# Kernel tuning notes

Hardware: AMD Instinct MI355X
Metric: run time of the kernel (lower is better)

## Reference

```python
import jax, jax.numpy as jnp
from jax import lax
import numpy as np


def _conv(x, w, b, groups=1):
    # x: NCHW, w: OIHW, stride 1, SAME padding
    y = lax.conv_general_dilated(x, w, (1, 1), 'SAME',
                                 dimension_numbers=('NCHW', 'OIHW', 'NCHW'),
                                 feature_group_count=groups)
    return y + b[None, :, None, None]


def setup_inputs() -> dict:
    key = jax.random.key(0)
    ks = jax.random.split(key, 9)
    B, C, H, W, N, K = 8, 64, 256, 256, 10, 64
    f = lambda k, s, sc=0.05: jax.random.normal(k, s, dtype=jnp.float32) * sc
    return dict(
        x=jax.random.normal(ks[0], (B, C, H, W), dtype=jnp.float32),
        ln_g=jnp.ones((C,), jnp.float32), ln_b=jnp.zeros((C,), jnp.float32),
        conv3_w=f(ks[1], (C, C, 3, 3)), conv3_b=jnp.zeros((C,), jnp.float32),
        dw_w=f(ks[2], (C, 1, 3, 3)), dw_b=jnp.zeros((C,), jnp.float32),
        c1_w=f(ks[3], (C, C, 1, 1)), c1_b=jnp.zeros((C,), jnp.float32),
        c2_w=f(ks[4], (N, C, 1, 1)), c2_b=jnp.zeros((N,), jnp.float32),
        base=f(ks[5], (N, K, K), 1.0),
        up_w=f(ks[6], (K, C, 3, 3)), up_b=jnp.zeros((K,), jnp.float32),
        down_w=f(ks[7], (C, K, 3, 3)), down_b=jnp.zeros((C,), jnp.float32),
    )


def reference(x, ln_g, ln_b, conv3_w, conv3_b, dw_w, dw_b, c1_w, c1_b,
              c2_w, c2_b, base, up_w, up_b, down_w, down_b):
    eps = 1e-5
    # LayerNorm over channel dim (permute(0,2,3,1) -> LN(last) -> permute back)
    mu = jnp.mean(x, axis=1, keepdims=True)
    var = jnp.var(x, axis=1, keepdims=True)
    xn = (x - mu) / jnp.sqrt(var + eps) * ln_g[None, :, None, None] + ln_b[None, :, None, None]
    x1 = jax.nn.gelu(_conv(xn, conv3_w, conv3_b), approximate=False)
    # predict module: dwconv -> GAP -> 1x1 -> relu -> 1x1 -> softmax over N
    C = x.shape[1]
    p = _conv(x1, dw_w, dw_b, groups=C)
    p = jnp.mean(p, axis=(2, 3), keepdims=True)           # [B,C,1,1]
    p = jax.nn.relu(_conv(p, c1_w, c1_b))
    p = _conv(p, c2_w, c2_b)[:, :, 0, 0]                  # [B,N]
    w = jax.nn.softmax(p, axis=1)                         # [B,N]
    # blend N basis KxK matrices per sample
    Wm = jnp.einsum('bn,nkl->bkl', w, base)               # [B,K,K]
    xm = _conv(x1, up_w, up_b)                            # [B,K,H,W]
    B, K, H, Wd = xm.shape
    xm = jnp.einsum('bkl,bkm->blm', Wm, xm.reshape(B, K, H * Wd)).reshape(B, K, H, Wd)
    xm = _conv(xm, down_w, down_b)                        # [B,C,H,W]
    return x + xm
```

## Files before the change

### kernel.cpp

```cpp
#include <hip/hip_runtime.h>
#include <math.h>

constexpr int B = 8, C = 64, H = 256, W = 256, HWc = H * W, N = 10;

typedef short bf8 __attribute__((ext_vector_type(8)));
typedef float f4  __attribute__((ext_vector_type(4)));
typedef unsigned short ushort;

__device__ __forceinline__ ushort f2bf(float f) {
  unsigned u = __builtin_bit_cast(unsigned, f);
  unsigned r = (u + 0x7fffu + ((u >> 16) & 1u)) >> 16;
  return (ushort)r;
}
__device__ __forceinline__ float bf2f(ushort h) {
  unsigned u = ((unsigned)h) << 16;
  return __builtin_bit_cast(float, u);
}

__global__ __launch_bounds__(256) void ln_k(
    const float* __restrict__ x, const float* __restrict__ g,
    const float* __restrict__ bt, ushort* __restrict__ xn) {
  int pix = blockIdx.x * 256 + threadIdx.x;
  int b = blockIdx.y;
  const float* xp = x + (size_t)b * C * HWc + pix;
  float v[64];
  float s = 0.f, s2 = 0.f;
#pragma unroll
  for (int c = 0; c < 64; c++) {
    v[c] = xp[(size_t)c * HWc];
    s += v[c]; s2 += v[c] * v[c];
  }
  float mu = s * (1.f / 64);
  float var = s2 * (1.f / 64) - mu * mu;
  float rstd = rsqrtf(var + 1e-5f);
  ushort* op = xn + ((size_t)b * HWc + pix) * 64;
#pragma unroll
  for (int ch = 0; ch < 8; ch++) {
    union { ushort us[8]; int4 v4; } pk;
#pragma unroll
    for (int j = 0; j < 8; j++) {
      int c = ch * 8 + j;
      pk.us[j] = f2bf((v[c] - mu) * rstd * g[c] + bt[c]);
    }
    *reinterpret_cast<int4*>(op + ch * 8) = pk.v4;
  }
}

__global__ void prep_w(const float* __restrict__ w3, const float* __restrict__ wu,
                       const float* __restrict__ wd, ushort* __restrict__ frags) {
  int idx = blockIdx.x * 256 + threadIdx.x;
  if (idx >= 3 * 4608) return;
  int conv = idx / 4608, r = idx % 4608;
  int s = r >> 8, cf = (r >> 6) & 3, lane = r & 63;
  const float* w = (conv == 0) ? w3 : (conv == 1) ? wu : wd;
  int co = (cf << 4) + (lane & 15);
  int tap = s >> 1;
  ushort* o = frags + conv * 36864 + ((size_t)r) * 8;
#pragma unroll
  for (int j = 0; j < 8; j++) {
    int ci = ((s & 1) << 5) + ((lane >> 4) << 3) + j;
    o[j] = f2bf(w[(co * 64 + ci) * 9 + tap]);
  }
}

struct Stg { int4 v[6]; };

__device__ __forceinline__ void stage_load(
    Stg& s, const ushort* __restrict__ in, int b, int h0, int w0,
    int ch2, int tid) {
#pragma unroll
  for (int it = 0; it < 6; it++) {
    int idx = it * 256 + tid;
    int4 v = make_int4(0, 0, 0, 0);
    if (idx < 1296) {
      int pix = idx >> 2, ch = idx & 3;
      int r = pix / 18, c = pix % 18;
      int gh = h0 + r - 1, gw = w0 + c - 1;
      if (gh >= 0 && gh < H && gw >= 0 && gw < W)
        v = *reinterpret_cast<const int4*>(
            in + (((size_t)b * H + gh) * W + gw) * 64 + ch2 * 32 + ch * 8);
    }
    s.v[it] = v;
  }
}

__device__ __forceinline__ void stage_write(const Stg& s, char* lds, int tid) {
#pragma unroll
  for (int it = 0; it < 6; it++) {
    int idx = it * 256 + tid;
    if (idx < 1296) {
      int pix = idx >> 2, ch = idx & 3;
      int c = pix % 18;
      int off = ((pix << 6) + (ch << 4)) ^ (((c >> 1) & 3) << 4);
      *reinterpret_cast<int4*>(lds + off) = s.v[it];
    }
  }
}

__device__ __forceinline__ void compute_half(
    const char* lds, const bf8* __restrict__ wf, int ch2,
    int wave, int lm, int lk, f4 (&acc)[16]) {
#pragma unroll
  for (int dx = 0; dx < 3; dx++) {
    bf8 wb3[3];
#pragma unroll
    for (int dy = 0; dy < 3; dy++) {
      int s = ((dy * 3 + dx) << 1) | ch2;
      wb3[dy] = wf[(s * 4 + wave) * 64 + (lk << 4) + lm];
    }
    int lc = lm + dx;
    int swz = ((lc >> 1) & 3) << 4;
#pragma unroll
    for (int hf = 0; hf < 2; hf++) {
      bf8 a[10];
#pragma unroll
      for (int r = 0; r < 10; r++) {
        int row = hf * 8 + r;
        int off = (((row * 18 + lc) << 6) + (lk << 4)) ^ swz;
        a[r] = *reinterpret_cast<const bf8*>(lds + off);
      }
#pragma unroll
      for (int dy = 0; dy < 3; dy++)
#pragma unroll
        for (int f = 0; f < 8; f++)
          acc[hf * 8 + f] =
              __builtin_amdgcn_mfma_f32_16x16x32_bf16(a[f + dy], wb3[dy], acc[hf * 8 + f], 0, 0, 0);
    }
  }
}

__device__ __forceinline__ void red_at(
    float* ldsf, const float (&a)[8], float* __restrict__ Ssum,
    int b, int tid) {
  __syncthreads();
#pragma unroll
  for (int j = 0; j < 8; j++) ldsf[j * 256 + tid] = a[j];
  __syncthreads();
  if (tid < 64) {
    float s = 0.f;
#pragma unroll
    for (int kk = 0; kk < 32; kk++) s += ldsf[(tid & 7) * 256 + kk * 8 + (tid >> 3)];
    atomicAdd(&Ssum[b * 64 + tid], s);
  }
}

template <int ACT, int OM, int DOST>
__global__ __launch_bounds__(256, 2) void conv_mfma(
    const ushort* __restrict__ in, const ushort* __restrict__ wfrag,
    const float* __restrict__ bias, const float* __restrict__ resid,
    ushort* __restrict__ outb, float* __restrict__ outf,
    float* __restrict__ Ssum) {
  __shared__ char lds[2 * 20736];
  char* ldsA = lds;
  char* ldsB = lds + 20736;
  int tid = threadIdx.x;
  int b = blockIdx.z;
  int h0 = blockIdx.y * 16, w0 = blockIdx.x * 16;
  int wave = tid >> 6, lane = tid & 63;
  int lm = lane & 15, lk = lane >> 4;
  const bf8* wf = reinterpret_cast<const bf8*>(wfrag);

  f4 acc[16];
  {
    float bv = bias[(wave << 4) + lm];
    f4 ini = {bv, bv, bv, bv};
#pragma unroll
    for (int f = 0; f < 16; f++) acc[f] = ini;
  }

  {
    Stg s0;
    stage_load(s0, in, b, h0, w0, 0, tid);
    stage_write(s0, ldsA, tid);
    __syncthreads();
  }
  {
    Stg s1;
    stage_load(s1, in, b, h0, w0, 1, tid);
    compute_half(ldsA, wf, 0, wave, lm, lk, acc);
    stage_write(s1, ldsB, tid);
    __syncthreads();
  }
  compute_half(ldsB, wf, 1, wave, lm, lk, acc);

  float* ldsf = reinterpret_cast<float*>(lds);
  if (OM == 0) {
    float s8[8];
    if (DOST) {
#pragma unroll
      for (int j = 0; j < 8; j++) s8[j] = 0.f;
    }
    for (int h2 = 0; h2 < 2; h2++) {
      __syncthreads();
#pragma unroll
      for (int fr = 0; fr < 8; fr++) {
        int f = h2 * 8 + fr;
        int co = (wave << 4) + lm;
#pragma unroll
        for (int r = 0; r < 4; r++) {
          int p = (lk << 2) + r;
          ldsf[fr * 1024 + p * 64 + (co ^ ((p & 12) << 2))] = acc[f][r];
        }
      }
      __syncthreads();
#pragma unroll
      for (int i = 0; i < 4; i++) {
        int q2 = i * 256 + tid;
        int co8 = q2 & 7, p = (q2 >> 3) & 15, fr = q2 >> 7;
        int cb = (co8 * 8) ^ ((p & 12) << 2);
        f4 v0 = *reinterpret_cast<f4*>(&ldsf[fr * 1024 + p * 64 + cb]);
        f4 v1 = *reinterpret_cast<f4*>(&ldsf[fr * 1024 + p * 64 + cb + 4]);
        float vv[8] = {v0[0], v0[1], v0[2], v0[3], v1[0], v1[1], v1[2], v1[3]};
        union { ushort us[8]; int4 i4; } pk;
#pragma unroll
        for (int j = 0; j < 8; j++) {
          float v = vv[j];
          if (ACT) v = 0.5f * v * (1.f + erff(v * 0.70710678118654752f));
          if (DOST) s8[j] += v;
          pk.us[j] = f2bf(v);
        }
        *reinterpret_cast<int4*>(
            outb + (((size_t)b * H + h0 + h2 * 8 + fr) * W + w0 + p) * 64 + co8 * 8) = pk.i4;
      }
    }
    if (DOST) red_at(ldsf, s8, Ssum, b, tid);
  } else {
    for (int h2 = 0; h2 < 2; h2++) {
      __syncthreads();
      if ((wave >> 1) == h2) {
        int co32 = ((wave & 1) << 4) + lm;
#pragma unroll
        for (int f = 0; f < 16; f++) {
          int pxl = (f << 4) + (lk << 2);
          int pxs = pxl ^ ((co32 & 7) << 2);
          *reinterpret_cast<f4*>(&ldsf[co32 * 256 + pxs]) = acc[f];
        }
      }
      float4 rv[8];
#pragma unroll
      for (int i = 0; i < 8; i++) {
        int q2 = i * 256 + tid;
        int chunk = q2 & 63, co32 = q2 >> 6;
        int pq = chunk * 4;
        int co = h2 * 32 + co32;
        size_t o = ((size_t)(b * 64 + co)) * HWc +
                   (size_t)(h0 + (pq >> 4)) * W + w0 + (pq & 15);
        rv[i] = *reinterpret_cast<const float4*>(resid + o);
      }
      __syncthreads();
#pragma unroll
      for (int i = 0; i < 8; i++) {
        int q2 = i * 256 + tid;
        int chunk = q2 & 63, co32 = q2 >> 6;
        int pq = chunk * 4;
        int pxs = pq ^ ((co32 & 7) << 2);
        f4 v = *reinterpret_cast<f4*>(&ldsf[co32 * 256 + pxs]);
        int co = h2 * 32 + co32;
        size_t o = ((size_t)(b * 64 + co)) * HWc +
                   (size_t)(h0 + (pq >> 4)) * W + w0 + (pq & 15);
        float4 ov;
        ov.x = v[0] + rv[i].x; ov.y = v[1] + rv[i].y;
        ov.z = v[2] + rv[i].z; ov.w = v[3] + rv[i].w;
        *reinterpret_cast<float4*>(outf + o) = ov;
      }
    }
  }
}

__global__ __launch_bounds__(256, 2) void upmix_mfma(
    const ushort* __restrict__ in, const ushort* __restrict__ wfrag,
    const float* __restrict__ bias, const ushort* __restrict__ wmf,
    ushort* __restrict__ out) {
  __shared__ char ldsS[20736];
  __shared__ char ldsX[32768];
  int tid = threadIdx.x;
  int b = blockIdx.z;
  int h0 = blockIdx.y * 16, w0 = blockIdx.x * 16;
  int wave = tid >> 6, lane = tid & 63;
  int lm = lane & 15, lk = lane >> 4;
  const bf8* wf = reinterpret_cast<const bf8*>(wfrag);

  const bf8* wmb = reinterpret_cast<const bf8*>(wmf + (size_t)b * 4096);
  bf8 wm[2];
#pragma unroll
  for (int s = 0; s < 2; s++) wm[s] = wmb[(s * 4 + wave) * 64 + lane];

  f4 acc[16];
  {
    float bv = bias[(wave << 4) + lm];
    f4 ini = {bv, bv, bv, bv};
#pragma unroll
    for (int f = 0; f < 16; f++) acc[f] = ini;
  }

  {
    Stg s0;
    stage_load(s0, in, b, h0, w0, 0, tid);
    stage_write(s0, ldsS, tid);
    __syncthreads();
  }
  {
    Stg s1;
    stage_load(s1, in, b, h0, w0, 1, tid);
    compute_half(ldsS, wf, 0, wave, lm, lk, acc);
    stage_write(s1, ldsX, tid);
    __syncthreads();
  }
  compute_half(ldsX, wf, 1, wave, lm, lk, acc);
  __syncthreads();

#pragma unroll
  for (int f = 0; f < 16; f++) {
#pragma unroll
    for (int r = 0; r < 4; r++) {
      int pc = (lk << 2) + r;
      int pix = (f << 4) + pc;
      int off = ((pix << 7) + ((wave << 4) + lm) * 2) ^ ((pc & 7) << 4);
      *reinterpret_cast<ushort*>(ldsX + off) = f2bf(acc[f][r]);
    }
  }
  __syncthreads();

  f4 acc2[16];
#pragma unroll
  for (int f = 0; f < 16; f++) acc2[f] = (f4){0.f, 0.f, 0.f, 0.f};
#pragma unroll
  for (int s = 0; s < 2; s++) {
    int kbyte = ((s << 5) + (lk << 3)) << 1;
#pragma unroll
    for (int f = 0; f < 16; f++) {
      int off = ((((f << 4) + lm) << 7) + kbyte) ^ ((lm & 7) << 4);
      bf8 a = *reinterpret_cast<const bf8*>(ldsX + off);
      acc2[f] = __builtin_amdgcn_mfma_f32_16x16x32_bf16(a, wm[s], acc2[f], 0, 0, 0);
    }
  }

  float* ldsf = reinterpret_cast<float*>(ldsX);
  for (int h2 = 0; h2 < 2; h2++) {
    __syncthreads();
#pragma unroll
    for (int fr = 0; fr < 8; fr++) {
      int f = h2 * 8 + fr;
      int co = (wave << 4) + lm;
#pragma unroll
      for (int r = 0; r < 4; r++) {
        int p = (lk << 2) + r;
        ldsf[fr * 1024 + p * 64 + (co ^ ((p & 12) << 2))] = acc2[f][r];
      }
    }
    __syncthreads();
#pragma unroll
    for (int i = 0; i < 4; i++) {
      int q2 = i * 256 + tid;
      int co8 = q2 & 7, p = (q2 >> 3) & 15, fr = q2 >> 7;
      int cb = (co8 * 8) ^ ((p & 12) << 2);
      f4 v0 = *reinterpret_cast<f4*>(&ldsf[fr * 1024 + p * 64 + cb]);
      f4 v1 = *reinterpret_cast<f4*>(&ldsf[fr * 1024 + p * 64 + cb + 4]);
      float vv[8] = {v0[0], v0[1], v0[2], v0[3], v1[0], v1[1], v1[2], v1[3]};
      union { ushort us[8]; int4 i4; } pk;
#pragma unroll
      for (int j = 0; j < 8; j++) pk.us[j] = f2bf(vv[j]);
      *reinterpret_cast<int4*>(
          out + (((size_t)b * H + h0 + h2 * 8 + fr) * W + w0 + p) * 64 + co8 * 8) = pk.i4;
    }
  }
}

__global__ __launch_bounds__(256) void mlp_k(
    const ushort* __restrict__ x1, const float* __restrict__ Ssum,
    const float* __restrict__ dww, const float* __restrict__ dwb,
    const float* __restrict__ c1w, const float* __restrict__ c1b,
    const float* __restrict__ c2w, const float* __restrict__ c2b,
    const float* __restrict__ basep, ushort* __restrict__ wmf) {
  int b = blockIdx.x;
  int t = threadIdx.x;
  __shared__ float red[256];
  __shared__ float eg[4][64], corn[4][64];
  __shared__ float pm[64], p1[64], p2[16];
  const size_t bb = (size_t)b * HWc * 64;
#pragma unroll
  for (int st = 0; st < 4; st++) {
    float s = 0.f;
    for (int i = 0; i < 64; i++) {
      int idx = i * 256 + t;
      int pix = idx >> 6, c = idx & 63;
      size_t off;
      if (st == 0)      off = ((size_t)pix) * 64 + c;
      else if (st == 1) off = ((size_t)(H - 1) * W + pix) * 64 + c;
      else if (st == 2) off = ((size_t)pix * W) * 64 + c;
      else              off = ((size_t)pix * W + (W - 1)) * 64 + c;
      s += bf2f(x1[bb + off]);
    }
    red[t] = s;
    __syncthreads();
    if (t < 64) eg[st][t] = red[t] + red[t + 64] + red[t + 128] + red[t + 192];
    __syncthreads();
  }
  if (t < 64) {
    corn[0][t] = bf2f(x1[bb + t]);
    corn[1][t] = bf2f(x1[bb + ((size_t)(W - 1)) * 64 + t]);
    corn[2][t] = bf2f(x1[bb + ((size_t)(H - 1) * W) * 64 + t]);
    corn[3][t] = bf2f(x1[bb + ((size_t)(H - 1) * W + W - 1) * 64 + t]);
  }
  __syncthreads();
  if (t < 64) {
    float S = Ssum[b * 64 + t];
    float R0 = eg[0][t], Rh = eg[1][t], C0 = eg[2][t], Cw = eg[3][t];
    float X00 = corn[0][t], X0w = corn[1][t], Xh0 = corn[2][t], Xhw = corn[3][t];
    float acc = 0.f;
#pragma unroll
    for (int ky = 0; ky < 3; ky++)
#pragma unroll
      for (int kx = 0; kx < 3; kx++) {
        float T = S;
        if (ky == 2) T -= R0;
        if (ky == 0) T -= Rh;
        if (kx == 2) T -= C0;
        if (kx == 0) T -= Cw;
        if (ky == 2 && kx == 2) T += X00;
        if (ky == 2 && kx == 0) T += X0w;
        if (ky == 0 && kx == 2) T += Xh0;
        if (ky == 0 && kx == 0) T += Xhw;
        acc += dww[t * 9 + ky * 3 + kx] * T;
      }
    pm[t] = acc * (1.f / HWc) + dwb[t];
  }
  __syncthreads();
  if (t < 64) {
    float a = c1b[t];
    for (int ci = 0; ci < 64; ci++) a += pm[ci] * c1w[t * 64 + ci];
    p1[t] = fmaxf(a, 0.f);
  }
  __syncthreads();
  if (t < N) {
    float a2 = c2b[t];
    for (int ci = 0; ci < 64; ci++) a2 += p1[ci] * c2w[t * 64 + ci];
    p2[t] = a2;
  }
  __syncthreads();
  float m = -1e30f;
  for (int n = 0; n < N; n++) m = fmaxf(m, p2[n]);
  float ev[N], s = 0.f;
  for (int n = 0; n < N; n++) { ev[n] = expf(p2[n] - m); s += ev[n]; }
  float inv = 1.f / s;
  for (int idx = t; idx < 4096; idx += 256) {
    int j = idx & 7, lane = (idx >> 3) & 63, cf = (idx >> 9) & 3, s2 = idx >> 11;
    int k = (s2 << 5) + ((lane >> 4) << 3) + j;
    int l = (cf << 4) + (lane & 15);
    float acc = 0.f;
    for (int n = 0; n < N; n++) acc += ev[n] * inv * basep[n * 4096 + k * 64 + l];
    wmf[(size_t)b * 4096 + idx] = f2bf(acc);
  }
}

__global__ void zero_k(float* p, int n) {
  int i = blockIdx.x * 256 + threadIdx.x;
  if (i < n) p[i] = 0.f;
}

extern "C" void kernel_launch(void* const* d_in, const int* in_sizes, int n_in,
                              void* d_out, int out_size, void* d_ws, size_t ws_size,
                              hipStream_t stream) {
  const float* x       = (const float*)d_in[0];
  const float* ln_g    = (const float*)d_in[1];
  const float* ln_b    = (const float*)d_in[2];
  const float* conv3_w = (const float*)d_in[3];
  const float* conv3_b = (const float*)d_in[4];
  const float* dw_w    = (const float*)d_in[5];
  const float* dw_b    = (const float*)d_in[6];
  const float* c1_w    = (const float*)d_in[7];
  const float* c1_b    = (const float*)d_in[8];
  const float* c2_w    = (const float*)d_in[9];
  const float* c2_b    = (const float*)d_in[10];
  const float* basep   = (const float*)d_in[11];
  const float* up_w    = (const float*)d_in[12];
  const float* up_b    = (const float*)d_in[13];
  const float* down_w  = (const float*)d_in[14];
  const float* down_b  = (const float*)d_in[15];
  float* out = (float*)d_out;

  char* wsb = (char*)d_ws;
  size_t big = (size_t)B * HWc * 64 * sizeof(ushort);
  ushort* bufA   = (ushort*)wsb;
  ushort* bufB   = (ushort*)(wsb + big);
  ushort* wfrags = (ushort*)(wsb + 2 * big);
  ushort* wmfrag = (ushort*)(wsb + 2 * big + 3 * 36864 * 2);
  float*  Ssum   = (float*)(wsb + 2 * big + 3 * 36864 * 2 + 8 * 4096 * 2);

  prep_w<<<54, 256, 0, stream>>>(conv3_w, up_w, down_w, wfrags);
  zero_k<<<2, 256, 0, stream>>>(Ssum, B * 64);
  ln_k<<<dim3(HWc / 256, B), 256, 0, stream>>>(x, ln_g, ln_b, bufA);
  conv_mfma<1, 0, 1><<<dim3(16, 16, B), 256, 0, stream>>>(
      bufA, wfrags + 0 * 36864, conv3_b, nullptr, bufB, nullptr, Ssum);
  mlp_k<<<B, 256, 0, stream>>>(bufB, Ssum, dw_w, dw_b, c1_w, c1_b, c2_w, c2_b,
                               basep, wmfrag);
  upmix_mfma<<<dim3(16, 16, B), 256, 0, stream>>>(
      bufB, wfrags + 1 * 36864, up_b, wmfrag, bufA);
  conv_mfma<0, 1, 0><<<dim3(16, 16, B), 256, 0, stream>>>(
      bufA, wfrags + 2 * 36864, down_b, x, nullptr, out, Ssum);
}
```

Measured before the change: 311.1 us.

## Stage conv input tiles directly into LDS via global_load_lds with zero buffer

```diff
diff --git a/kernel.cpp b/kernel.cpp
--- a/kernel.cpp
+++ b/kernel.cpp
@@ -63,37 +63,27 @@
   }
 }
 
-struct Stg { int4 v[6]; };
-
-__device__ __forceinline__ void stage_load(
-    Stg& s, const ushort* __restrict__ in, int b, int h0, int w0,
-    int ch2, int tid) {
+typedef __attribute__((address_space(3))) unsigned lds_u32;
+typedef __attribute__((address_space(1))) const unsigned glb_u32;
+
+__device__ __forceinline__ void stage_gll(
+    char* ldsbuf, const ushort* __restrict__ in, const ushort* __restrict__ zbuf,
+    int b, int h0, int w0, int ch2, int tid) {
+  int wave = tid >> 6, lane = tid & 63;
 #pragma unroll
   for (int it = 0; it < 6; it++) {
-    int idx = it * 256 + tid;
-    int4 v = make_int4(0, 0, 0, 0);
-    if (idx < 1296) {
-      int pix = idx >> 2, ch = idx & 3;
-      int r = pix / 18, c = pix % 18;
-      int gh = h0 + r - 1, gw = w0 + c - 1;
-      if (gh >= 0 && gh < H && gw >= 0 && gw < W)
-        v = *reinterpret_cast<const int4*>(
-            in + (((size_t)b * H + gh) * W + gw) * 64 + ch2 * 32 + ch * 8);
-    }
-    s.v[it] = v;
-  }
-}
-
-__device__ __forceinline__ void stage_write(const Stg& s, char* lds, int tid) {
-#pragma unroll
-  for (int it = 0; it < 6; it++) {
-    int idx = it * 256 + tid;
-    if (idx < 1296) {
-      int pix = idx >> 2, ch = idx & 3;
-      int c = pix % 18;
-      int off = ((pix << 6) + (ch << 4)) ^ (((c >> 1) & 3) << 4);
-      *reinterpret_cast<int4*>(lds + off) = s.v[it];
-    }
+    int idx = it * 256 + wave * 64 + lane;
+    int pix = idx >> 2, ch = idx & 3;
+    int r = pix / 18, c = pix % 18;
+    int gh = h0 + r - 1, gw = w0 + c - 1;
+    int chs = ch ^ ((c >> 1) & 3);
+    bool ok = (idx < 1296) && (gh >= 0) && (gh < H) && (gw >= 0) && (gw < W);
+    const ushort* src = ok
+        ? in + (((size_t)b * H + gh) * W + gw) * 64 + ch2 * 32 + chs * 8
+        : zbuf;
+    char* dst = ldsbuf + (it * 256 + wave * 64) * 16;
+    __builtin_amdgcn_global_load_lds((glb_u32*)(const void*)src,
+                                     (lds_u32*)(void*)dst, 16, 0, 0);
   }
 }
 
@@ -128,6 +118,18 @@
     }
   }
 }
+
+#define STAGE_PIPELINE(bufA_, bufB_)                                      \
+  stage_gll(bufA_, in, zbuf, b, h0, w0, 0, tid);                          \
+  stage_gll(bufB_, in, zbuf, b, h0, w0, 1, tid);                          \
+  asm volatile("s_waitcnt vmcnt(6)" ::: "memory");                        \
+  __builtin_amdgcn_s_barrier();                                           \
+  __builtin_amdgcn_sched_barrier(0);                                      \
+  compute_half(bufA_, wf, 0, wave, lm, lk, acc);                          \
+  asm volatile("s_waitcnt vmcnt(0)" ::: "memory");                        \
+  __builtin_amdgcn_s_barrier();                                           \
+  __builtin_amdgcn_sched_barrier(0);                                      \
+  compute_half(bufB_, wf, 1, wave, lm, lk, acc);
 
 __device__ __forceinline__ void red_at(
     float* ldsf, const float (&a)[8], float* __restrict__ Ssum,
@@ -149,10 +151,10 @@
     const ushort* __restrict__ in, const ushort* __restrict__ wfrag,
     const float* __restrict__ bias, const float* __restrict__ resid,
     ushort* __restrict__ outb, float* __restrict__ outf,
-    float* __restrict__ Ssum) {
-  __shared__ char lds[2 * 20736];
+    float* __restrict__ Ssum, const ushort* __restrict__ zbuf) {
+  __shared__ char lds[2 * 24576];
   char* ldsA = lds;
-  char* ldsB = lds + 20736;
+  char* ldsB = lds + 24576;
   int tid = threadIdx.x;
   int b = blockIdx.z;
   int h0 = blockIdx.y * 16, w0 = blockIdx.x * 16;
@@ -168,20 +170,7 @@
     for (int f = 0; f < 16; f++) acc[f] = ini;
   }
 
-  {
-    Stg s0;
-    stage_load(s0, in, b, h0, w0, 0, tid);
-    stage_write(s0, ldsA, tid);
-    __syncthreads();
-  }
-  {
-    Stg s1;
-    stage_load(s1, in, b, h0, w0, 1, tid);
-    compute_half(ldsA, wf, 0, wave, lm, lk, acc);
-    stage_write(s1, ldsB, tid);
-    __syncthreads();
-  }
-  compute_half(ldsB, wf, 1, wave, lm, lk, acc);
+  STAGE_PIPELINE(ldsA, ldsB)
 
   float* ldsf = reinterpret_cast<float*>(lds);
   if (OM == 0) {
@@ -270,8 +259,8 @@
 __global__ __launch_bounds__(256, 2) void upmix_mfma(
     const ushort* __restrict__ in, const ushort* __restrict__ wfrag,
     const float* __restrict__ bias, const ushort* __restrict__ wmf,
-    ushort* __restrict__ out) {
-  __shared__ char ldsS[20736];
+    ushort* __restrict__ out, const ushort* __restrict__ zbuf) {
+  __shared__ char ldsS[24576];
   __shared__ char ldsX[32768];
   int tid = threadIdx.x;
   int b = blockIdx.z;
@@ -293,20 +282,7 @@
     for (int f = 0; f < 16; f++) acc[f] = ini;
   }
 
-  {
-    Stg s0;
-    stage_load(s0, in, b, h0, w0, 0, tid);
-    stage_write(s0, ldsS, tid);
-    __syncthreads();
-  }
-  {
-    Stg s1;
-    stage_load(s1, in, b, h0, w0, 1, tid);
-    compute_half(ldsS, wf, 0, wave, lm, lk, acc);
-    stage_write(s1, ldsX, tid);
-    __syncthreads();
-  }
-  compute_half(ldsX, wf, 1, wave, lm, lk, acc);
+  STAGE_PIPELINE(ldsS, ldsX)
   __syncthreads();
 
 #pragma unroll
@@ -486,16 +462,17 @@
   ushort* wfrags = (ushort*)(wsb + 2 * big);
   ushort* wmfrag = (ushort*)(wsb + 2 * big + 3 * 36864 * 2);
   float*  Ssum   = (float*)(wsb + 2 * big + 3 * 36864 * 2 + 8 * 4096 * 2);
+  const ushort* zbuf = (const ushort*)(Ssum + 512);
 
   prep_w<<<54, 256, 0, stream>>>(conv3_w, up_w, down_w, wfrags);
-  zero_k<<<2, 256, 0, stream>>>(Ssum, B * 64);
+  zero_k<<<8, 256, 0, stream>>>(Ssum, 2048);
   ln_k<<<dim3(HWc / 256, B), 256, 0, stream>>>(x, ln_g, ln_b, bufA);
   conv_mfma<1, 0, 1><<<dim3(16, 16, B), 256, 0, stream>>>(
-      bufA, wfrags + 0 * 36864, conv3_b, nullptr, bufB, nullptr, Ssum);
+      bufA, wfrags + 0 * 36864, conv3_b, nullptr, bufB, nullptr, Ssum, zbuf);
   mlp_k<<<B, 256, 0, stream>>>(bufB, Ssum, dw_w, dw_b, c1_w, c1_b, c2_w, c2_b,
                                basep, wmfrag);
   upmix_mfma<<<dim3(16, 16, B), 256, 0, stream>>>(
-      bufB, wfrags + 1 * 36864, up_b, wmfrag, bufA);
+      bufB, wfrags + 1 * 36864, up_b, wmfrag, bufA, zbuf);
   conv_mfma<0, 1, 0><<<dim3(16, 16, B), 256, 0, stream>>>(
-      bufA, wfrags + 2 * 36864, down_b, x, nullptr, out, Ssum);
-}
+      bufA, wfrags + 2 * 36864, down_b, x, nullptr, out, Ssum, zbuf);
+}
```

New measurement: 302.7 us. -2.7%, faster.
